# Kernel optimization log

Measured on AMD Instinct MI355X. Metric: run time of the kernel, lower is better.

The kernel has to match this reference:

```python
import jax, jax.numpy as jnp
import numpy as np
from jax import lax

EPS = 1e-3  # BatchNorm4d eps


def conv4d(x, w, b):
    """4D conv (VALID, stride 1) via kt-shifted 3D convolutions.
    x: [B, Cin, T, D, H, W]; w: [Cout, Cin, kt, kd, kh, kw]; b: [Cout].
    Returns [B, Cout, T', D', H', W']."""
    B, C, T = x.shape[0], x.shape[1], x.shape[2]
    kt = w.shape[2]
    T_out = T - kt + 1
    acc = 0.0
    for i in range(kt):  # tiny fixed loop over kernel's first spatial dim
        xs = x[:, :, i:i + T_out]                              # [B,C,T_out,D,H,W]
        xs = jnp.transpose(xs, (0, 2, 1, 3, 4, 5))             # [B,T_out,C,D,H,W]
        xs = xs.reshape(B * T_out, C, *x.shape[3:])            # fold T_out into batch
        y = lax.conv_general_dilated(
            xs, w[:, :, i], window_strides=(1, 1, 1), padding='VALID',
            dimension_numbers=('NCDHW', 'OIDHW', 'NCDHW'))
        acc = acc + y                                          # [B*T_out,Cout,D',H',W']
    O = w.shape[0]
    y = acc.reshape(B, T_out, O, *acc.shape[2:])
    y = jnp.transpose(y, (0, 2, 1, 3, 4, 5))                   # [B,Cout,T',D',H',W']
    return y + b[None, :, None, None, None, None]


def setup_inputs() -> dict:
    key = jax.random.key(0)
    k = jax.random.split(key, 7)
    Cin, filters, ks = 4, 3, 3
    Cmid, Cout = Cin * filters, Cin * filters * filters        # 12, 36
    x = jax.random.normal(k[0], (8, Cin, 20, 24, 24, 24), dtype=jnp.float32)
    W1 = jax.random.normal(k[1], (Cmid, Cin, ks, ks, ks, ks), dtype=jnp.float32) * 0.05
    b1 = jax.random.normal(k[2], (Cmid,), dtype=jnp.float32) * 0.05
    gamma = jnp.ones((Cmid,), dtype=jnp.float32)
    beta = jnp.zeros((Cmid,), dtype=jnp.float32)
    W2 = jax.random.normal(k[3], (Cout, Cmid, ks, ks, ks, ks), dtype=jnp.float32) * 0.05
    b2 = jax.random.normal(k[4], (Cout,), dtype=jnp.float32) * 0.05
    return {"x": x, "W1": W1, "b1": b1, "gamma": gamma, "beta": beta,
            "W2": W2, "b2": b2}


def reference(x, W1, b1, gamma, beta, W2, b2):
    h = jax.nn.relu(conv4d(x, W1, b1))                         # conv1 -> ReLU
    # BatchNorm4d (training mode: batch statistics over B and all 4 spatial dims)
    mean = jnp.mean(h, axis=(0, 2, 3, 4, 5), keepdims=True)
    var = jnp.var(h, axis=(0, 2, 3, 4, 5), keepdims=True)
    g = gamma[None, :, None, None, None, None]
    bb = beta[None, :, None, None, None, None]
    h = (h - mean) * jax.lax.rsqrt(var + EPS) * g + bb
    h = jax.nn.relu(conv4d(h, W2, b2))                         # conv2 -> ReLU
    return h.reshape(h.shape[0], -1)                           # flatten
```

## Files before the change

kernel.cpp:

```cpp
#include <hip/hip_runtime.h>

#define EPS 0.001f

typedef __attribute__((ext_vector_type(8))) short bf16x8;
typedef __attribute__((ext_vector_type(4))) short bf16x4;
typedef __attribute__((ext_vector_type(4))) float f32x4;

constexpr int Bn = 8, Tx = 20, Dx = 24, Hx = 24, Wx = 24;
constexpr int Cmid = 12, CoutN = 36;
constexpr int T1 = 18, D1 = 22;
constexpr int T2 = 16, D2 = 20;

constexpr int SXD = 576, SXT = 13824, SXC = 276480;
constexpr long SXB = 1105920;

constexpr int XTD = 2304, XTT = 55296;
constexpr long XTB = (long)Tx * XTT;

constexpr int HTW = 16;
constexpr int HTH = 22 * 16;
constexpr int HTD = 22 * 22 * 16;
constexpr int HTT = 22 * HTD;
constexpr long HTB = (long)T1 * HTT;

constexpr int S2D = 400, S2T = 8000, S2O = 128000;
constexpr long S2B = 4608000;

constexpr int NBLK1 = 8 * 18 * 22;

__device__ __forceinline__ unsigned short f2bf(float f) {
    unsigned u = __builtin_bit_cast(unsigned, f);
    u = (u + 0x7fffu + ((u >> 16) & 1u)) >> 16;
    return (unsigned short)u;
}

__global__ __launch_bounds__(576) void k_xt(const float* __restrict__ x,
                                            unsigned short* __restrict__ xt) {
    const int tid = threadIdx.x;
    const int d = blockIdx.x, t = blockIdx.y, b = blockIdx.z;
    const float* src = x + (long)b * SXB + (long)t * SXT + (long)d * SXD + tid;
    float v0 = src[0];
    float v1 = src[SXC];
    float v2 = src[2 * SXC];
    float v3 = src[3 * SXC];
    uint2 p;
    p.x = (unsigned)f2bf(v0) | ((unsigned)f2bf(v1) << 16);
    p.y = (unsigned)f2bf(v2) | ((unsigned)f2bf(v3) << 16);
    *(uint2*)(xt + (long)b * XTB + (long)t * XTT + (long)d * XTD + tid * 4) = p;
}

__global__ void k_finW1(const float* __restrict__ W1, unsigned short* __restrict__ Wf1) {
    const int p = blockIdx.x;
    const int lane = threadIdx.x;
    const int m = lane & 15;
    const int q = lane >> 4;
    unsigned short vals[8];
#pragma unroll
    for (int j = 0; j < 8; ++j) {
        int kk = q * 8 + j;
        int g = 2 * p + (kk >> 4);
        int r = kk & 15;
        int kw = r >> 2, cin = r & 3;
        float v = 0.f;
        if (m < 12 && kw < 3 && g < 27) {
            int kt = g / 9, g9 = g - kt * 9, kd = g9 / 3, kh = g9 - kd * 3;
            v = W1[m * 324 + cin * 81 + kt * 27 + kd * 9 + kh * 3 + kw];
        }
        vals[j] = f2bf(v);
    }
    uint4 pk;
    pk.x = (unsigned)vals[0] | ((unsigned)vals[1] << 16);
    pk.y = (unsigned)vals[2] | ((unsigned)vals[3] << 16);
    pk.z = (unsigned)vals[4] | ((unsigned)vals[5] << 16);
    pk.w = (unsigned)vals[6] | ((unsigned)vals[7] << 16);
    *(uint4*)(Wf1 + p * 512 + lane * 8) = pk;
}

__global__ __launch_bounds__(512, 4) void k_conv1m(
    const unsigned short* __restrict__ xt, const unsigned short* __restrict__ Wf1,
    const float* __restrict__ b1, unsigned short* __restrict__ h1t,
    float* __restrict__ part)
{
    __shared__ char lds[9 * 4608 + 16];
    __shared__ float ssum[8][12], ssq[8][12];

    const int tid  = threadIdx.x;
    const int lane = tid & 63;
    const int wv   = tid >> 6;
    const int d = blockIdx.x;
    const int t = blockIdx.y;
    const int b = blockIdx.z;
    const int bid = (b * 18 + t) * 22 + d;

    const int n16 = lane & 15;
    const int q   = lane >> 4;

    {
        for (int i = tid; i < 2592; i += 512) {
            int p = i / 288, r = i - p * 288;
            int kt = p / 3, kd = p - kt * 3;
            const unsigned short* src = xt + (long)b * XTB + (long)(t + kt) * XTT
                                      + (long)(d + kd) * XTD + r * 8;
            *(uint4*)(lds + i * 16) = *(const uint4*)src;
        }
    }

    bf16x8 A[14];
#pragma unroll
    for (int p = 0; p < 14; ++p)
        A[p] = *(const bf16x8*)(Wf1 + p * 512 + lane * 8);

    int hh[4], ww[4], nn[4];
#pragma unroll
    for (int u = 0; u < 4; ++u) {
        int n = (wv * 4 + u) * 16 + n16;
        nn[u] = n;
        int nc = n < 484 ? n : 483;
        hh[u] = nc / 22;
        ww[u] = nc - hh[u] * 22;
    }

    f32x4 acc[4];
#pragma unroll
    for (int u = 0; u < 4; ++u) acc[u] = (f32x4){0.f, 0.f, 0.f, 0.f};

    __syncthreads();

#pragma unroll
    for (int p = 0; p < 14; ++p) {
        int gq = 2 * p + (q >> 1);
        int gc = gq < 27 ? gq : 26;
        int kt = gc / 9, g9 = gc - kt * 9, kd = g9 / 3, kh = g9 - kd * 3;
        const int off = (kt * 3 + kd) * 4608 + kh * 192 + (q & 1) * 16;
#pragma unroll
        for (int u = 0; u < 4; ++u) {
            const int addr = off + hh[u] * 192 + ww[u] * 8;
            bf16x4 lo = *(const bf16x4*)(lds + addr);
            bf16x4 hi = *(const bf16x4*)(lds + addr + 8);
            bf16x8 bb;
            bb[0] = lo[0]; bb[1] = lo[1]; bb[2] = lo[2]; bb[3] = lo[3];
            bb[4] = hi[0]; bb[5] = hi[1]; bb[6] = hi[2]; bb[7] = hi[3];
            acc[u] = __builtin_amdgcn_mfma_f32_16x16x32_bf16(A[p], bb, acc[u], 0, 0, 0);
        }
    }

    const int c0 = q * 4;
    float bias[4];
#pragma unroll
    for (int r = 0; r < 4; ++r) bias[r] = (c0 + r) < 12 ? b1[c0 + r] : 0.f;

    float ls[4] = {0.f, 0.f, 0.f, 0.f}, lq[4] = {0.f, 0.f, 0.f, 0.f};
#pragma unroll
    for (int u = 0; u < 4; ++u) {
        const bool valid = nn[u] < 484;
        float v[4];
#pragma unroll
        for (int r = 0; r < 4; ++r) {
            float val = fmaxf(acc[u][r] + bias[r], 0.f);
            v[r] = val;
            if (valid) { ls[r] += val; lq[r] += val * val; }
        }
        if (valid) {
            const long ob = (long)b * HTB + (long)t * HTT + (long)d * HTD
                          + (long)hh[u] * HTH + (long)ww[u] * HTW + c0;
            uint2 pk;
            pk.x = (unsigned)f2bf(v[0]) | ((unsigned)f2bf(v[1]) << 16);
            pk.y = (unsigned)f2bf(v[2]) | ((unsigned)f2bf(v[3]) << 16);
            *(uint2*)(h1t + ob) = pk;
        }
    }

#pragma unroll
    for (int off = 8; off > 0; off >>= 1) {
#pragma unroll
        for (int r = 0; r < 4; ++r) {
            ls[r] += __shfl_xor(ls[r], off);
            lq[r] += __shfl_xor(lq[r], off);
        }
    }
    if (n16 == 0 && q < 3) {
#pragma unroll
        for (int r = 0; r < 4; ++r) {
            ssum[wv][c0 + r] = ls[r];
            ssq[wv][c0 + r] = lq[r];
        }
    }
    __syncthreads();
    if (tid < 12) {
        float s = 0.f;
#pragma unroll
        for (int i = 0; i < 8; ++i) s += ssum[i][tid];
        part[bid * 24 + tid] = s;
    } else if (tid < 24) {
        float s = 0.f;
#pragma unroll
        for (int i = 0; i < 8; ++i) s += ssq[i][tid - 12];
        part[bid * 24 + tid] = s;
    }
}

__global__ void k_red(const float* __restrict__ part, float* __restrict__ stats2) {
    __shared__ float s[256];
    const int c = blockIdx.x;
    const int tid = threadIdx.x;
    float acc = 0.f;
    for (int i = tid; i < NBLK1; i += 256) acc += part[i * 24 + c];
    s[tid] = acc;
    __syncthreads();
    for (int off = 128; off > 0; off >>= 1) {
        if (tid < off) s[tid] += s[tid + off];
        __syncthreads();
    }
    if (tid == 0) stats2[c] = s[0];
}

__global__ void k_fin1(const float* __restrict__ stats2, const float* __restrict__ gamma,
                       const float* __restrict__ beta, const float* __restrict__ W2,
                       const float* __restrict__ b2, float* __restrict__ abuf,
                       float* __restrict__ b2ws)
{
    __shared__ float a_s[12], d_s[12];
    const int tid = threadIdx.x;
    if (tid < 12) {
        const float N = 1533312.f;
        float mean = stats2[tid] / N;
        float var  = stats2[12 + tid] / N - mean * mean;
        float a = gamma[tid] * rsqrtf(var + EPS);
        abuf[tid] = a_s[tid] = a;
        d_s[tid] = beta[tid] - mean * a;
    }
    __syncthreads();
    if (tid < 36) {
        float s = b2[tid];
        for (int c = 0; c < 12; ++c) {
            const float* p = W2 + tid * 972 + c * 81;
            float tsum = 0.f;
            for (int k = 0; k < 81; ++k) tsum += p[k];
            s += d_s[c] * tsum;
        }
        b2ws[tid] = s;
    }
}

__global__ void k_fin2(const float* __restrict__ W2, const float* __restrict__ abuf,
                       unsigned short* __restrict__ Wf)
{
    const int bi = blockIdx.x;
    const int lane = threadIdx.x;
    const int ch = bi & 1;
    const int tmp = bi >> 1;
    const int mt = tmp % 3;
    const int g = tmp / 3;
    const int kt = g / 9, g9 = g % 9, kd = g9 / 3, kh = g9 % 3;
    const int o = mt * 16 + (lane & 15);

    unsigned short vals[8];
#pragma unroll
    for (int j = 0; j < 8; ++j) {
        int k = ch * 32 + ((lane >> 4) << 3) + j;
        float v = 0.f;
        if (k < 48 && o < 36) {
            int kw = k >> 4, c = k & 15;
            if (c < 12)
                v = W2[o * 972 + c * 81 + kt * 27 + kd * 9 + kh * 3 + kw] * abuf[c];
        }
        vals[j] = f2bf(v);
    }
    uint4 pk;
    pk.x = (unsigned)vals[0] | ((unsigned)vals[1] << 16);
    pk.y = (unsigned)vals[2] | ((unsigned)vals[3] << 16);
    pk.z = (unsigned)vals[4] | ((unsigned)vals[5] << 16);
    pk.w = (unsigned)vals[6] | ((unsigned)vals[7] << 16);
    *(uint4*)(Wf + bi * 512 + lane * 8) = pk;
}

__global__ __launch_bounds__(320, 3) void k_conv2m(
    const unsigned short* __restrict__ h1t, const unsigned short* __restrict__ Wf,
    const float* __restrict__ b2ws, float* __restrict__ out)
{
    __shared__ char lds[3 * 15488];

    const int tid  = threadIdx.x;
    const int lane = tid & 63;
    const int wv   = tid >> 6;
    const int d = blockIdx.x;
    const int t = blockIdx.y;
    const int b = blockIdx.z;

    const int n16 = lane & 15;
    const int q   = lane >> 4;

    int posbase[5], pb[5];
#pragma unroll
    for (int u = 0; u < 5; ++u) {
        int p = (wv * 5 + u) * 16 + n16;
        int h = p / 20, w = p - h * 20;
        pb[u] = p;
        posbase[u] = h * 704 + w * 16;
    }
    const int qoff0 = (q & 1) * 352 + (q >> 1) * 16;
    const int qoff1 = (q & 1) * 352 + 32;

    f32x4 acc[5][3];
#pragma unroll
    for (int u = 0; u < 5; ++u)
#pragma unroll
        for (int mt = 0; mt < 3; ++mt)
            acc[u][mt] = (f32x4){0.f, 0.f, 0.f, 0.f};

    for (int kt = 0; kt < 3; ++kt) {
        __syncthreads();
        {
            const unsigned short* src = h1t + (long)b * HTB + (long)(t + kt) * HTT
                                      + (long)d * HTD;
            for (int i = tid; i < 2904; i += 320) {
                int pl = i / 968; int r = i - pl * 968;
                int h = r / 44; int r2 = r - h * 44;
                int w = r2 >> 1, chh = r2 & 1;
                int dst = pl * 968 + h * 44 + chh * 22 + w;
                *(uint4*)(lds + dst * 16) = *(const uint4*)(src + i * 8);
            }
        }
        __syncthreads();

        for (int g9 = 0; g9 < 9; ++g9) {
            const int kd = g9 / 3, kh = g9 - kd * 3;
            const int g = kt * 9 + g9;

            bf16x8 A[3][2];
#pragma unroll
            for (int mt = 0; mt < 3; ++mt)
#pragma unroll
                for (int c2 = 0; c2 < 2; ++c2)
                    A[mt][c2] = *(const bf16x8*)(Wf + (((g * 3 + mt) * 2 + c2) << 9) + lane * 8);

            const int goff = kd * 15488 + kh * 704;
#pragma unroll
            for (int u = 0; u < 5; ++u) {
                bf16x8 b0 = *(const bf16x8*)(lds + posbase[u] + goff + qoff0);
                bf16x8 b1 = *(const bf16x8*)(lds + posbase[u] + goff + qoff1);
#pragma unroll
                for (int mt = 0; mt < 3; ++mt) {
                    acc[u][mt] = __builtin_amdgcn_mfma_f32_16x16x32_bf16(A[mt][0], b0, acc[u][mt], 0, 0, 0);
                    acc[u][mt] = __builtin_amdgcn_mfma_f32_16x16x32_bf16(A[mt][1], b1, acc[u][mt], 0, 0, 0);
                }
            }
        }
    }

    const long ob = (long)b * S2B + (long)t * S2T + (long)d * S2D;
#pragma unroll
    for (int mt = 0; mt < 3; ++mt)
#pragma unroll
    for (int r = 0; r < 4; ++r) {
        const int o = mt * 16 + q * 4 + r;
        if (o < 36) {
            const float bias = b2ws[o];
#pragma unroll
            for (int u = 0; u < 5; ++u)
                out[ob + (long)o * S2O + pb[u]] = fmaxf(acc[u][mt][r] + bias, 0.f);
        }
    }
}

extern "C" void kernel_launch(void* const* d_in, const int* in_sizes, int n_in,
                              void* d_out, int out_size, void* d_ws, size_t ws_size,
                              hipStream_t stream) {
    const float* x     = (const float*)d_in[0];
    const float* W1    = (const float*)d_in[1];
    const float* b1    = (const float*)d_in[2];
    const float* gamma = (const float*)d_in[3];
    const float* beta  = (const float*)d_in[4];
    const float* W2    = (const float*)d_in[5];
    const float* b2    = (const float*)d_in[6];
    float* out = (float*)d_out;

    float* ws     = (float*)d_ws;
    float* stats2 = ws;
    float* abuf   = ws + 32;
    float* b2ws   = ws + 64;
    unsigned short* Wf1 = (unsigned short*)((char*)d_ws + 1024);
    unsigned short* Wf  = (unsigned short*)((char*)d_ws + 16384);
    float* part   = (float*)((char*)d_ws + 196608);
    unsigned short* h1t = (unsigned short*)((char*)d_ws + 524288);
    unsigned short* xt  = (unsigned short*)((char*)d_ws + 50331648);

    k_xt<<<dim3(24, 20, 8), 576, 0, stream>>>(x, xt);
    k_finW1<<<14, 64, 0, stream>>>(W1, Wf1);
    k_conv1m<<<dim3(22, 18, 8), 512, 0, stream>>>(xt, Wf1, b1, h1t, part);
    k_red<<<24, 256, 0, stream>>>(part, stats2);
    k_fin1<<<1, 64, 0, stream>>>(stats2, gamma, beta, W2, b2, abuf, b2ws);
    k_fin2<<<162, 64, 0, stream>>>(W2, abuf, Wf);
    k_conv2m<<<dim3(20, 16, 8), 320, 0, stream>>>(h1t, Wf, b2ws, out);
}
```

Baseline: 511.3 us.

## Use direct global-to-LDS loads, swizzle block order, prefetch weights, transpose partials

Several unrelated changes land together. conv2 now stages h1t tiles with global_load_lds DMA instead of register round-trips, which changes the LDS layout and B-operand offsets. conv2 also software-prefetches the next tap's weight fragments into registers. Both conv kernels move to a 1D grid with an XCD-aware block swizzle so neighbouring tiles share L2. The BN partial sums are stored channel-major so the reduction reads coalesced, and k_fin1 parallelises the W2 tap sums across 432 threads. The risks are a wrong LDS layout remap and extra register pressure from the doubled A fragments.

After: 450.4 us. 1.14x faster.

```diff
diff --git a/kernel.cpp b/kernel.cpp
--- a/kernel.cpp
+++ b/kernel.cpp
@@ -32,6 +32,12 @@
     unsigned u = __builtin_bit_cast(unsigned, f);
     u = (u + 0x7fffu + ((u >> 16) & 1u)) >> 16;
     return (unsigned short)u;
+}
+
+__device__ __forceinline__ void gload16(const void* g, void* l) {
+    __builtin_amdgcn_global_load_lds(
+        (const __attribute__((address_space(1))) void*)g,
+        (__attribute__((address_space(3))) void*)l, 16, 0, 0);
 }
 
 __global__ __launch_bounds__(576) void k_xt(const float* __restrict__ x,
@@ -87,9 +93,13 @@
     const int tid  = threadIdx.x;
     const int lane = tid & 63;
     const int wv   = tid >> 6;
-    const int d = blockIdx.x;
-    const int t = blockIdx.y;
-    const int b = blockIdx.z;
+
+    const int l  = blockIdx.x;
+    const int sw = (l & 7) * 396 + (l >> 3);
+    const int d  = sw % 22;
+    const int tt = sw / 22;
+    const int t  = tt % 18;
+    const int b  = tt / 18;
     const int bid = (b * 18 + t) * 22 + d;
 
     const int n16 = lane & 15;
@@ -190,12 +200,12 @@
         float s = 0.f;
 #pragma unroll
         for (int i = 0; i < 8; ++i) s += ssum[i][tid];
-        part[bid * 24 + tid] = s;
+        part[tid * NBLK1 + bid] = s;
     } else if (tid < 24) {
         float s = 0.f;
 #pragma unroll
         for (int i = 0; i < 8; ++i) s += ssq[i][tid - 12];
-        part[bid * 24 + tid] = s;
+        part[tid * NBLK1 + bid] = s;
     }
 }
 
@@ -204,7 +214,7 @@
     const int c = blockIdx.x;
     const int tid = threadIdx.x;
     float acc = 0.f;
-    for (int i = tid; i < NBLK1; i += 256) acc += part[i * 24 + c];
+    for (int i = tid; i < NBLK1; i += 256) acc += part[c * NBLK1 + i];
     s[tid] = acc;
     __syncthreads();
     for (int off = 128; off > 0; off >>= 1) {
@@ -219,25 +229,31 @@
                        const float* __restrict__ b2, float* __restrict__ abuf,
                        float* __restrict__ b2ws)
 {
-    __shared__ float a_s[12], d_s[12];
+    __shared__ float d_s[12];
+    __shared__ float red[36][12];
     const int tid = threadIdx.x;
     if (tid < 12) {
         const float N = 1533312.f;
         float mean = stats2[tid] / N;
         float var  = stats2[12 + tid] / N - mean * mean;
         float a = gamma[tid] * rsqrtf(var + EPS);
-        abuf[tid] = a_s[tid] = a;
+        abuf[tid] = a;
         d_s[tid] = beta[tid] - mean * a;
+    }
+    __syncthreads();
+    if (tid < 432) {
+        const int o = tid / 12, c = tid - o * 12;
+        const float* p = W2 + o * 972 + c * 81;
+        float ts = 0.f;
+#pragma unroll
+        for (int k = 0; k < 81; ++k) ts += p[k];
+        red[o][c] = d_s[c] * ts;
     }
     __syncthreads();
     if (tid < 36) {
         float s = b2[tid];
-        for (int c = 0; c < 12; ++c) {
-            const float* p = W2 + tid * 972 + c * 81;
-            float tsum = 0.f;
-            for (int k = 0; k < 81; ++k) tsum += p[k];
-            s += d_s[c] * tsum;
-        }
+#pragma unroll
+        for (int c = 0; c < 12; ++c) s += red[tid][c];
         b2ws[tid] = s;
     }
 }
@@ -278,28 +294,32 @@
     const unsigned short* __restrict__ h1t, const unsigned short* __restrict__ Wf,
     const float* __restrict__ b2ws, float* __restrict__ out)
 {
-    __shared__ char lds[3 * 15488];
+    __shared__ char lds[2944 * 16];
 
     const int tid  = threadIdx.x;
     const int lane = tid & 63;
     const int wv   = tid >> 6;
-    const int d = blockIdx.x;
-    const int t = blockIdx.y;
-    const int b = blockIdx.z;
+
+    const int l  = blockIdx.x;
+    const int sw = (l & 7) * 320 + (l >> 3);
+    const int d  = sw % 20;
+    const int tq = sw / 20;
+    const int t  = tq & 15;
+    const int b  = tq >> 4;
 
     const int n16 = lane & 15;
     const int q   = lane >> 4;
 
-    int posbase[5], pb[5];
+    int posb[5], pb[5];
 #pragma unroll
     for (int u = 0; u < 5; ++u) {
         int p = (wv * 5 + u) * 16 + n16;
         int h = p / 20, w = p - h * 20;
         pb[u] = p;
-        posbase[u] = h * 704 + w * 16;
-    }
-    const int qoff0 = (q & 1) * 352 + (q >> 1) * 16;
-    const int qoff1 = (q & 1) * 352 + 32;
+        posb[u] = h * 704 + w * 32;
+    }
+    const int qb0 = q * 16;
+    const int qb1 = (q & 1) * 16 + 64;
 
     f32x4 acc[5][3];
 #pragma unroll
@@ -307,44 +327,58 @@
 #pragma unroll
         for (int mt = 0; mt < 3; ++mt)
             acc[u][mt] = (f32x4){0.f, 0.f, 0.f, 0.f};
+
+    bf16x8 A0[3][2];
+#pragma unroll
+    for (int mt = 0; mt < 3; ++mt)
+#pragma unroll
+        for (int c2 = 0; c2 < 2; ++c2)
+            A0[mt][c2] = *(const bf16x8*)(Wf + ((mt * 2 + c2) << 9) + lane * 8);
 
     for (int kt = 0; kt < 3; ++kt) {
         __syncthreads();
         {
             const unsigned short* src = h1t + (long)b * HTB + (long)(t + kt) * HTT
                                       + (long)d * HTD;
-            for (int i = tid; i < 2904; i += 320) {
-                int pl = i / 968; int r = i - pl * 968;
-                int h = r / 44; int r2 = r - h * 44;
-                int w = r2 >> 1, chh = r2 & 1;
-                int dst = pl * 968 + h * 44 + chh * 22 + w;
-                *(uint4*)(lds + dst * 16) = *(const uint4*)(src + i * 8);
+#pragma unroll
+            for (int r = 0; r < 9; ++r) {
+                const int u0 = r * 320 + wv * 64;
+                gload16(src + (long)(u0 + lane) * 8, lds + u0 * 16);
             }
+            if (wv == 0)
+                gload16(src + (long)(2880 + lane) * 8, lds + 2880 * 16);
         }
         __syncthreads();
 
         for (int g9 = 0; g9 < 9; ++g9) {
+            const int g  = kt * 9 + g9;
+            const int gn = (g < 26) ? g + 1 : 26;
             const int kd = g9 / 3, kh = g9 - kd * 3;
-            const int g = kt * 9 + g9;
-
-            bf16x8 A[3][2];
+            const int goff = kd * 15488 + kh * 704;
+
+            bf16x8 A1[3][2];
 #pragma unroll
             for (int mt = 0; mt < 3; ++mt)
 #pragma unroll
                 for (int c2 = 0; c2 < 2; ++c2)
-                    A[mt][c2] = *(const bf16x8*)(Wf + (((g * 3 + mt) * 2 + c2) << 9) + lane * 8);
-
-            const int goff = kd * 15488 + kh * 704;
+                    A1[mt][c2] = *(const bf16x8*)(Wf + (((gn * 3 + mt) * 2 + c2) << 9) + lane * 8);
+
 #pragma unroll
             for (int u = 0; u < 5; ++u) {
-                bf16x8 b0 = *(const bf16x8*)(lds + posbase[u] + goff + qoff0);
-                bf16x8 b1 = *(const bf16x8*)(lds + posbase[u] + goff + qoff1);
+                const char* bbase = lds + posb[u] + goff;
+                bf16x8 b0 = *(const bf16x8*)(bbase + qb0);
+                bf16x8 b1 = *(const bf16x8*)(bbase + qb1);
 #pragma unroll
                 for (int mt = 0; mt < 3; ++mt) {
-                    acc[u][mt] = __builtin_amdgcn_mfma_f32_16x16x32_bf16(A[mt][0], b0, acc[u][mt], 0, 0, 0);
-                    acc[u][mt] = __builtin_amdgcn_mfma_f32_16x16x32_bf16(A[mt][1], b1, acc[u][mt], 0, 0, 0);
+                    acc[u][mt] = __builtin_amdgcn_mfma_f32_16x16x32_bf16(A0[mt][0], b0, acc[u][mt], 0, 0, 0);
+                    acc[u][mt] = __builtin_amdgcn_mfma_f32_16x16x32_bf16(A0[mt][1], b1, acc[u][mt], 0, 0, 0);
                 }
             }
+#pragma unroll
+            for (int mt = 0; mt < 3; ++mt)
+#pragma unroll
+                for (int c2 = 0; c2 < 2; ++c2)
+                    A0[mt][c2] = A1[mt][c2];
         }
     }
 
@@ -387,9 +421,9 @@
 
     k_xt<<<dim3(24, 20, 8), 576, 0, stream>>>(x, xt);
     k_finW1<<<14, 64, 0, stream>>>(W1, Wf1);
-    k_conv1m<<<dim3(22, 18, 8), 512, 0, stream>>>(xt, Wf1, b1, h1t, part);
+    k_conv1m<<<3168, 512, 0, stream>>>(xt, Wf1, b1, h1t, part);
     k_red<<<24, 256, 0, stream>>>(part, stats2);
-    k_fin1<<<1, 64, 0, stream>>>(stats2, gamma, beta, W2, b2, abuf, b2ws);
+    k_fin1<<<1, 512, 0, stream>>>(stats2, gamma, beta, W2, b2, abuf, b2ws);
     k_fin2<<<162, 64, 0, stream>>>(W2, abuf, Wf);
-    k_conv2m<<<dim3(20, 16, 8), 320, 0, stream>>>(h1t, Wf, b2ws, out);
-}
+    k_conv2m<<<2560, 320, 0, stream>>>(h1t, Wf, b2ws, out);
+}
```
